# Optimization experiments

Hardware: AMD Instinct MI355X
Metric: run time of the kernel (lower is better)

Reference implementation:

```python
import jax, jax.numpy as jnp
import numpy as np

N, D, H, E, A = 524288, 64, 128, 8, 18
BN_EPS = 1e-5


def setup_inputs() -> dict:
    key = jax.random.key(0)
    ks = jax.random.split(key, 4)
    X = jax.random.normal(ks[0], (N, D), dtype=jnp.float32)
    W1 = jax.random.normal(ks[1], (H, D), dtype=jnp.float32) * 0.05
    b1 = jnp.zeros((H,), dtype=jnp.float32)
    gamma = jnp.ones((H,), dtype=jnp.float32)
    beta = jnp.zeros((H,), dtype=jnp.float32)
    rmean = jnp.zeros((H,), dtype=jnp.float32)
    rvar = jnp.ones((H,), dtype=jnp.float32)
    W2 = jax.random.normal(ks[2], (E, H), dtype=jnp.float32) * 0.05
    b2 = jnp.zeros((E,), dtype=jnp.float32)
    We = jax.random.normal(ks[3], (E, A, D), dtype=jnp.float32) * 0.05
    return {"X": X, "W1": W1, "b1": b1, "gamma": gamma, "beta": beta,
            "rmean": rmean, "rvar": rvar, "W2": W2, "b2": b2, "We": We}


def reference(X, W1, b1, gamma, beta, rmean, rvar, W2, b2, We):
    # Gating MLP: Linear -> BatchNorm1d (eval, running stats) -> ReLU -> Linear
    h = X @ W1.T + b1                                   # [N, H]
    h = gamma * (h - rmean) * jax.lax.rsqrt(rvar + BN_EPS) + beta
    h = jax.nn.relu(h)
    logits = h @ W2.T + b2                              # [N, E]
    # Straight-through hard routing
    y_soft = jax.nn.softmax(logits, axis=-1)
    y_hard = jax.nn.one_hot(jnp.argmax(y_soft, axis=-1), E, dtype=y_soft.dtype)
    ret = y_hard - jax.lax.stop_gradient(y_soft) + y_soft  # [N, E]
    # All experts at once: [N,E,A], then mask-weighted sum over experts
    expert_out = jnp.einsum('nd,ead->nea', X, We)
    output = jnp.einsum('nea,ne->na', expert_out, ret)     # [N, A]
    return output, ret
```

## Files before the change

### kernel.cpp

```cpp
#include <hip/hip_runtime.h>
#include <hip/hip_bf16.h>
#include <math.h>

#define DD 64
#define HH 128
#define EE 8
#define AA 18
#define BN_EPS 1e-5f

#define TIE_MARGIN 5e-5f

#define WE_STRIDE 1156

__global__ __launch_bounds__(256, 4) void moe_router_kernel(
    const float* __restrict__ X,
    const float* __restrict__ W1,
    const float* __restrict__ b1,
    const float* __restrict__ gamma,
    const float* __restrict__ beta,
    const float* __restrict__ rmean,
    const float* __restrict__ rvar,
    const float* __restrict__ W2,
    const float* __restrict__ b2,
    const float* __restrict__ We,
    float* __restrict__ out,
    float* __restrict__ ret,
    int Ntot)
{
    __shared__ float sWe[EE * WE_STRIDE];

    const int tid = threadIdx.x;
    const int n = blockIdx.x * 256 + tid;

    for (int i = tid; i < EE * AA * DD; i += 256) {
        int e = i / (AA * DD);
        int r = i - e * (AA * DD);
        sWe[e * WE_STRIDE + r] = We[i];
    }

    float4 x[16];
    if (n < Ntot) {
        const float4* xv = (const float4*)(X + (size_t)n * DD);
        #pragma unroll
        for (int k = 0; k < 16; ++k) x[k] = xv[k];
    }

    __syncthreads();

    if (n >= Ntot) return;

    float logits[EE];
    #pragma unroll
    for (int e = 0; e < EE; ++e) logits[e] = b2[e];

    #pragma unroll 2
    for (int j = 0; j < HH; ++j) {
        const float4* wv = (const float4*)(W1 + j * DD);
        float s0 = 0.f, s1 = 0.f, s2 = 0.f, s3 = 0.f;
        #pragma unroll
        for (int k = 0; k < 16; ++k) {
            float4 w = wv[k];
            s0 = fmaf(x[k].x, w.x, s0);
            s1 = fmaf(x[k].y, w.y, s1);
            s2 = fmaf(x[k].z, w.z, s2);
            s3 = fmaf(x[k].w, w.w, s3);
        }
        float h = ((s0 + s1) + (s2 + s3)) + b1[j];
        float sc = gamma[j] * rsqrtf(rvar[j] + BN_EPS);
        float hb = fmaf(h - rmean[j], sc, beta[j]);
        hb = fmaxf(hb, 0.f);
        #pragma unroll
        for (int e = 0; e < EE; ++e)
            logits[e] = fmaf(hb, W2[e * HH + j], logits[e]);
    }

    int emax = 0;
    float lmax = logits[0];
    #pragma unroll
    for (int e = 1; e < EE; ++e) {
        if (logits[e] > lmax) { lmax = logits[e]; emax = e; }
    }
    float second = -INFINITY;
    #pragma unroll
    for (int e = 0; e < EE; ++e) {
        if (e != emax && logits[e] > second) second = logits[e];
    }

    if (lmax - second < TIE_MARGIN) {
        const float* xg = X + (size_t)n * DD;
        double ld[EE];
        #pragma unroll
        for (int e = 0; e < EE; ++e) ld[e] = (double)b2[e];
        for (int j = 0; j < HH; ++j) {
            const float* w = W1 + j * DD;
            double hd = 0.0;
            for (int k = 0; k < DD; ++k)
                hd += (double)xg[k] * (double)w[k];
            hd += (double)b1[j];
            double sc = (double)gamma[j] / sqrt((double)rvar[j] + 1e-5);
            double hb = (hd - (double)rmean[j]) * sc + (double)beta[j];
            hb = hb > 0.0 ? hb : 0.0;
            #pragma unroll
            for (int e = 0; e < EE; ++e)
                ld[e] += hb * (double)W2[e * HH + j];
        }
        emax = 0;
        double lm = ld[0];
        #pragma unroll
        for (int e = 1; e < EE; ++e) {
            if (ld[e] > lm) { lm = ld[e]; emax = e; }
        }
    }

    float4* retv = (float4*)(ret + (size_t)n * EE);
    retv[0] = make_float4(emax == 0 ? 1.f : 0.f, emax == 1 ? 1.f : 0.f,
                          emax == 2 ? 1.f : 0.f, emax == 3 ? 1.f : 0.f);
    retv[1] = make_float4(emax == 4 ? 1.f : 0.f, emax == 5 ? 1.f : 0.f,
                          emax == 6 ? 1.f : 0.f, emax == 7 ? 1.f : 0.f);

    const float* wexp = &sWe[emax * WE_STRIDE];
    float outv[AA];
    #pragma unroll
    for (int a = 0; a < AA; ++a) {
        const float4* wv = (const float4*)(wexp + a * DD);
        float s0 = 0.f, s1 = 0.f, s2 = 0.f, s3 = 0.f;
        #pragma unroll
        for (int k = 0; k < 16; ++k) {
            float4 w = wv[k];
            s0 = fmaf(x[k].x, w.x, s0);
            s1 = fmaf(x[k].y, w.y, s1);
            s2 = fmaf(x[k].z, w.z, s2);
            s3 = fmaf(x[k].w, w.w, s3);
        }
        outv[a] = (s0 + s1) + (s2 + s3);
    }
    float2* ov = (float2*)(out + (size_t)n * AA);
    #pragma unroll
    for (int a2 = 0; a2 < 9; ++a2)
        ov[a2] = make_float2(outv[2 * a2], outv[2 * a2 + 1]);
}

extern "C" void kernel_launch(void* const* d_in, const int* in_sizes, int n_in,
                              void* d_out, int out_size, void* d_ws, size_t ws_size,
                              hipStream_t stream) {
    const float* X     = (const float*)d_in[0];
    const float* W1    = (const float*)d_in[1];
    const float* b1    = (const float*)d_in[2];
    const float* gamma = (const float*)d_in[3];
    const float* beta  = (const float*)d_in[4];
    const float* rmean = (const float*)d_in[5];
    const float* rvar  = (const float*)d_in[6];
    const float* W2    = (const float*)d_in[7];
    const float* b2    = (const float*)d_in[8];
    const float* We    = (const float*)d_in[9];

    const int Ntot = in_sizes[0] / DD;
    float* out = (float*)d_out;
    float* ret = out + (size_t)Ntot * AA;

    const int nblocks = (Ntot + 255) / 256;
    moe_router_kernel<<<nblocks, 256, 0, stream>>>(
        X, W1, b1, gamma, beta, rmean, rvar, W2, b2, We, out, ret, Ntot);
}
```

Before: 780.9 us.

## Split rare double-precision tie recheck into a separate fixup kernel

Moves the double-precision near-tie recomputation out of the main kernel into a second kernel that runs only for rows flagged in a workspace buffer, and rewrites their ret and out. The main kernel loses the divergent fp64 branch, which should reduce register pressure and code size. It also hoists the X loads ahead of the shared-memory We fill and lowers the launch-bounds occupancy hint from 4 to 2. In exchange it adds a second launch, a per-row flag write and a full flag read, plus a redundant first write for flagged rows.

Result: no change. 795.7 us (+1.9%).

```diff
diff --git a/kernel.cpp b/kernel.cpp
--- a/kernel.cpp
+++ b/kernel.cpp
@@ -12,7 +12,7 @@
 
 #define WE_STRIDE 1156
 
-__global__ __launch_bounds__(256, 4) void moe_router_kernel(
+__global__ __launch_bounds__(256, 2) void moe_hot(
     const float* __restrict__ X,
     const float* __restrict__ W1,
     const float* __restrict__ b1,
@@ -25,24 +25,25 @@
     const float* __restrict__ We,
     float* __restrict__ out,
     float* __restrict__ ret,
+    int* __restrict__ flags,
     int Ntot)
 {
     __shared__ float sWe[EE * WE_STRIDE];
 
     const int tid = threadIdx.x;
     const int n = blockIdx.x * 256 + tid;
+
+    float4 x[16];
+    if (n < Ntot) {
+        const float4* xv = (const float4*)(X + (size_t)n * DD);
+        #pragma unroll
+        for (int k = 0; k < 16; ++k) x[k] = xv[k];
+    }
 
     for (int i = tid; i < EE * AA * DD; i += 256) {
         int e = i / (AA * DD);
         int r = i - e * (AA * DD);
         sWe[e * WE_STRIDE + r] = We[i];
-    }
-
-    float4 x[16];
-    if (n < Ntot) {
-        const float4* xv = (const float4*)(X + (size_t)n * DD);
-        #pragma unroll
-        for (int k = 0; k < 16; ++k) x[k] = xv[k];
     }
 
     __syncthreads();
@@ -85,32 +86,7 @@
     for (int e = 0; e < EE; ++e) {
         if (e != emax && logits[e] > second) second = logits[e];
     }
-
-    if (lmax - second < TIE_MARGIN) {
-        const float* xg = X + (size_t)n * DD;
-        double ld[EE];
-        #pragma unroll
-        for (int e = 0; e < EE; ++e) ld[e] = (double)b2[e];
-        for (int j = 0; j < HH; ++j) {
-            const float* w = W1 + j * DD;
-            double hd = 0.0;
-            for (int k = 0; k < DD; ++k)
-                hd += (double)xg[k] * (double)w[k];
-            hd += (double)b1[j];
-            double sc = (double)gamma[j] / sqrt((double)rvar[j] + 1e-5);
-            double hb = (hd - (double)rmean[j]) * sc + (double)beta[j];
-            hb = hb > 0.0 ? hb : 0.0;
-            #pragma unroll
-            for (int e = 0; e < EE; ++e)
-                ld[e] += hb * (double)W2[e * HH + j];
-        }
-        emax = 0;
-        double lm = ld[0];
-        #pragma unroll
-        for (int e = 1; e < EE; ++e) {
-            if (ld[e] > lm) { lm = ld[e]; emax = e; }
-        }
-    }
+    flags[n] = (lmax - second < TIE_MARGIN) ? 1 : 0;
 
     float4* retv = (float4*)(ret + (size_t)n * EE);
     retv[0] = make_float4(emax == 0 ? 1.f : 0.f, emax == 1 ? 1.f : 0.f,
@@ -119,6 +95,84 @@
                           emax == 6 ? 1.f : 0.f, emax == 7 ? 1.f : 0.f);
 
     const float* wexp = &sWe[emax * WE_STRIDE];
+    float outv[AA];
+    #pragma unroll
+    for (int a = 0; a < AA; ++a) {
+        const float4* wv = (const float4*)(wexp + a * DD);
+        float s0 = 0.f, s1 = 0.f, s2 = 0.f, s3 = 0.f;
+        #pragma unroll
+        for (int k = 0; k < 16; ++k) {
+            float4 w = wv[k];
+            s0 = fmaf(x[k].x, w.x, s0);
+            s1 = fmaf(x[k].y, w.y, s1);
+            s2 = fmaf(x[k].z, w.z, s2);
+            s3 = fmaf(x[k].w, w.w, s3);
+        }
+        outv[a] = (s0 + s1) + (s2 + s3);
+    }
+    float2* ov = (float2*)(out + (size_t)n * AA);
+    #pragma unroll
+    for (int a2 = 0; a2 < 9; ++a2)
+        ov[a2] = make_float2(outv[2 * a2], outv[2 * a2 + 1]);
+}
+
+__global__ __launch_bounds__(256, 2) void moe_fix(
+    const float* __restrict__ X,
+    const float* __restrict__ W1,
+    const float* __restrict__ b1,
+    const float* __restrict__ gamma,
+    const float* __restrict__ beta,
+    const float* __restrict__ rmean,
+    const float* __restrict__ rvar,
+    const float* __restrict__ W2,
+    const float* __restrict__ b2,
+    const float* __restrict__ We,
+    float* __restrict__ out,
+    float* __restrict__ ret,
+    const int* __restrict__ flags,
+    int Ntot)
+{
+    const int n = blockIdx.x * 256 + threadIdx.x;
+    if (n >= Ntot) return;
+    if (flags[n] == 0) return;
+
+    const float* xg = X + (size_t)n * DD;
+
+    double ld[EE];
+    #pragma unroll
+    for (int e = 0; e < EE; ++e) ld[e] = (double)b2[e];
+    for (int j = 0; j < HH; ++j) {
+        const float* w = W1 + j * DD;
+        double hd = 0.0;
+        for (int k = 0; k < DD; ++k)
+            hd += (double)xg[k] * (double)w[k];
+        hd += (double)b1[j];
+        double sc = (double)gamma[j] / sqrt((double)rvar[j] + 1e-5);
+        double hb = (hd - (double)rmean[j]) * sc + (double)beta[j];
+        hb = hb > 0.0 ? hb : 0.0;
+        #pragma unroll
+        for (int e = 0; e < EE; ++e)
+            ld[e] += hb * (double)W2[e * HH + j];
+    }
+    int emax = 0;
+    double lm = ld[0];
+    #pragma unroll
+    for (int e = 1; e < EE; ++e) {
+        if (ld[e] > lm) { lm = ld[e]; emax = e; }
+    }
+
+    float4* retv = (float4*)(ret + (size_t)n * EE);
+    retv[0] = make_float4(emax == 0 ? 1.f : 0.f, emax == 1 ? 1.f : 0.f,
+                          emax == 2 ? 1.f : 0.f, emax == 3 ? 1.f : 0.f);
+    retv[1] = make_float4(emax == 4 ? 1.f : 0.f, emax == 5 ? 1.f : 0.f,
+                          emax == 6 ? 1.f : 0.f, emax == 7 ? 1.f : 0.f);
+
+    float4 x[16];
+    const float4* xv = (const float4*)xg;
+    #pragma unroll
+    for (int k = 0; k < 16; ++k) x[k] = xv[k];
+
+    const float* wexp = We + (size_t)emax * AA * DD;
     float outv[AA];
     #pragma unroll
     for (int a = 0; a < AA; ++a) {
@@ -157,8 +211,11 @@
     const int Ntot = in_sizes[0] / DD;
     float* out = (float*)d_out;
     float* ret = out + (size_t)Ntot * AA;
+    int* flags = (int*)d_ws;
 
     const int nblocks = (Ntot + 255) / 256;
-    moe_router_kernel<<<nblocks, 256, 0, stream>>>(
-        X, W1, b1, gamma, beta, rmean, rvar, W2, b2, We, out, ret, Ntot);
+    moe_hot<<<nblocks, 256, 0, stream>>>(
+        X, W1, b1, gamma, beta, rmean, rvar, W2, b2, We, out, ret, flags, Ntot);
+    moe_fix<<<nblocks, 256, 0, stream>>>(
+        X, W1, b1, gamma, beta, rmean, rvar, W2, b2, We, out, ret, flags, Ntot);
 }
```
